# Kernel tuning notes

Hardware: AMD Instinct MI355X
Metric: run time of the kernel (lower is better)

The kernel has to match this reference:

```python
import jax, jax.numpy as jnp
import numpy as np

B, D, N_CLASSES = 8192, 256, 64
MARGIN = 0.5


def setup_inputs() -> dict:
    key = jax.random.key(0)
    k1, k2 = jax.random.split(key)
    emb = jax.random.normal(k1, (B, D), dtype=jnp.float32)
    emb = emb / jnp.linalg.norm(emb, axis=1, keepdims=True)  # module expects L2-normalised
    labels = jax.random.randint(k2, (B,), 0, N_CLASSES)
    return {"embeddings": emb, "labels": labels}


def _pairwise_dist(x):
    # torch.cdist(x, x, p=2): sqrt of clamped squared distances, safe at 0 for grads
    sq = jnp.sum(x * x, axis=1)
    d2 = jnp.maximum(sq[:, None] + sq[None, :] - 2.0 * (x @ x.T), 0.0)
    safe = jnp.where(d2 > 0.0, d2, 1.0)
    return jnp.where(d2 > 0.0, jnp.sqrt(safe), 0.0)


def reference(embeddings, labels):
    # Vectorized semi-hard mining: for each anchor,
    #   d_ap = max positive distance; the mined negative is the MIN negative
    #   distance (argmin over the semi-hard subset == global neg argmin when
    #   that min is < d_ap + margin; otherwise the subset is empty -> skip).
    dist = _pairwise_dist(embeddings)            # [B, B]
    n = labels.shape[0]
    same = labels[:, None] == labels[None, :]
    eye = jnp.eye(n, dtype=bool)
    pos_mask = same & ~eye
    neg_mask = ~same

    NEG = jnp.float32(-1e30)
    POS = jnp.float32(1e30)
    d_ap = jnp.max(jnp.where(pos_mask, dist, NEG), axis=1)   # hardest positive
    d_an = jnp.min(jnp.where(neg_mask, dist, POS), axis=1)   # closest negative

    has_pos = jnp.any(pos_mask, axis=1)
    has_neg = jnp.any(neg_mask, axis=1)
    valid = has_pos & has_neg & (d_an < d_ap + MARGIN)       # semi-hard exists

    losses = jax.nn.relu(d_ap - d_an + MARGIN)
    count = jnp.sum(valid)
    total = jnp.sum(jnp.where(valid, losses, 0.0))
    zero = jnp.sum(embeddings) * 0.0
    return jnp.where(count > 0, total / jnp.maximum(count, 1).astype(losses.dtype), zero)
```

## Files before the change

### kernel.cpp

```cpp
#include <hip/hip_runtime.h>
#include <hip/hip_bf16.h>

#define Bn 8192
#define Dn 256
#define MARGIN_F 0.5f

typedef short short8 __attribute__((ext_vector_type(8)));
typedef float floatx4 __attribute__((ext_vector_type(4)));

__device__ inline unsigned short f2bf(float f) {
    unsigned int u = __float_as_uint(f);
    unsigned int r = (u + 0x7fffu + ((u >> 16) & 1u)) >> 16;
    return (unsigned short)r;
}

#define OFF_SQ   ((size_t)Bn * Dn * 2)
#define OFF_POS  (OFF_SQ + Bn * 4)
#define OFF_NEG  (OFF_POS + Bn * 4)
#define OFF_ACC  (OFF_NEG + Bn * 4)

__global__ __launch_bounds__(256) void prep_kernel(
        const float* __restrict__ emb, unsigned short* __restrict__ embT,
        float* __restrict__ sq, unsigned int* __restrict__ posb,
        unsigned int* __restrict__ negb, unsigned int* __restrict__ accs) {
    const int w = threadIdx.x >> 6;
    const int lane = threadIdx.x & 63;
    const int row = blockIdx.x * 4 + w;

    const float4 v = *(const float4*)(emb + (size_t)row * Dn + lane * 4);
    float ss = v.x * v.x + v.y * v.y + v.z * v.z + v.w * v.w;
    #pragma unroll
    for (int m = 32; m >= 1; m >>= 1) ss += __shfl_xor(ss, m);

    uint2 o;
    o.x = (unsigned int)f2bf(v.x) | ((unsigned int)f2bf(v.y) << 16);
    o.y = (unsigned int)f2bf(v.z) | ((unsigned int)f2bf(v.w) << 16);
    const int kg = lane >> 1;
    *(uint2*)(embT + ((size_t)kg * Bn + row) * 8 + (lane & 1) * 4) = o;

    if (lane == 0) {
        sq[row] = ss;
        posb[row] = 0u;
        negb[row] = 0xFFFFFFFFu;
    }
    if (blockIdx.x == 0 && threadIdx.x == 0) {
        accs[0] = 0u; accs[1] = 0u; accs[2] = 0u;
    }
}

__global__ __launch_bounds__(256, 2) void mine_kernel(
        const unsigned short* __restrict__ embT, const float* __restrict__ sq,
        const int* __restrict__ labels, unsigned int* __restrict__ posb,
        unsigned int* __restrict__ negb) {
    const int tid  = threadIdx.x;
    const int w    = tid >> 6;
    const int lane = tid & 63;
    const int quad = lane >> 4;
    const int c    = lane & 15;

    const int iBase  = blockIdx.x * 256 + w * 64;
    const int jSplit = blockIdx.y * 512;

    const size_t KS = (size_t)4 * Bn * 8;

    short8 aFrag[4][8];
    #pragma unroll
    for (int m = 0; m < 4; ++m) {
        const unsigned short* ap = embT + ((size_t)quad * Bn + iBase + m * 16 + c) * 8;
        #pragma unroll
        for (int ks = 0; ks < 8; ++ks)
            aFrag[m][ks] = *(const short8*)(ap + ks * KS);
    }
    int labI[4][4];
    #pragma unroll
    for (int m = 0; m < 4; ++m)
        #pragma unroll
        for (int r = 0; r < 4; ++r)
            labI[m][r] = labels[iBase + m * 16 + quad * 4 + r];

    float rpos[4][4], rneg[4][4];
    #pragma unroll
    for (int m = 0; m < 4; ++m)
        #pragma unroll
        for (int r = 0; r < 4; ++r) { rpos[m][r] = -1e30f; rneg[m][r] = 1e30f; }

    for (int jt = 0; jt < 16; ++jt) {
        #pragma unroll
        for (int n = 0; n < 2; ++n) {
            const int jRow = jSplit + jt * 32 + n * 16 + c;
            const unsigned short* bp = embT + ((size_t)quad * Bn + jRow) * 8;
            const float sj = sq[jRow];
            const int   lj = labels[jRow];
            floatx4 acc[4];
            #pragma unroll
            for (int m = 0; m < 4; ++m) acc[m] = (floatx4){0.f, 0.f, 0.f, 0.f};
            #pragma unroll
            for (int kc = 0; kc < 2; ++kc) {
                short8 bF[4];
                #pragma unroll
                for (int k4 = 0; k4 < 4; ++k4)
                    bF[k4] = *(const short8*)(bp + (kc * 4 + k4) * KS);
                #pragma unroll
                for (int k4 = 0; k4 < 4; ++k4)
                    #pragma unroll
                    for (int m = 0; m < 4; ++m)
                        acc[m] = __builtin_amdgcn_mfma_f32_16x16x32_bf16(
                            aFrag[m][kc * 4 + k4], bF[k4], acc[m], 0, 0, 0);
            }
            #pragma unroll
            for (int m = 0; m < 4; ++m)
                #pragma unroll
                for (int r = 0; r < 4; ++r) {
                    float s = fmaf(-2.0f, acc[m][r], sj);
                    bool  e = (lj == labI[m][r]);
                    rpos[m][r] = e ? fmaxf(rpos[m][r], s) : rpos[m][r];
                    rneg[m][r] = e ? rneg[m][r] : fminf(rneg[m][r], s);
                }
        }
    }

    #pragma unroll
    for (int m = 0; m < 4; ++m)
        #pragma unroll
        for (int r = 0; r < 4; ++r) {
            float p = rpos[m][r], q = rneg[m][r];
            #pragma unroll
            for (int msk = 1; msk <= 8; msk <<= 1) {
                p = fmaxf(p, __shfl_xor(p, msk));
                q = fminf(q, __shfl_xor(q, msk));
            }
            if (c == 0) {
                int ig = iBase + m * 16 + quad * 4 + r;
                if (p > -1e29f) atomicMax(&posb[ig], __float_as_uint(p + 4.0f));
                if (q <  1e29f) atomicMin(&negb[ig], __float_as_uint(q + 4.0f));
            }
        }
}

__global__ __launch_bounds__(256) void finalize_kernel(
        const float* __restrict__ sq, const unsigned int* __restrict__ posb,
        const unsigned int* __restrict__ negb, float* __restrict__ accsF,
        unsigned int* __restrict__ accsU, float* __restrict__ out) {
    const int i = blockIdx.x * 256 + threadIdx.x;
    unsigned int pb = posb[i], nb = negb[i];
    bool hp = (pb != 0u);
    bool hn = (nb != 0xFFFFFFFFu);
    float si  = sq[i];
    float dap = sqrtf(fmaxf(si + (__uint_as_float(pb) - 4.0f), 0.0f));
    float dan = sqrtf(fmaxf(si + (__uint_as_float(nb) - 4.0f), 0.0f));
    bool valid = hp && hn && (dan < dap + MARGIN_F);
    float t  = valid ? fmaxf(dap - dan + MARGIN_F, 0.0f) : 0.0f;
    float cc = valid ? 1.0f : 0.0f;
    #pragma unroll
    for (int m = 32; m >= 1; m >>= 1) {
        t  += __shfl_xor(t, m);
        cc += __shfl_xor(cc, m);
    }
    __shared__ float sT[4], sC[4];
    int w = threadIdx.x >> 6, lane = threadIdx.x & 63;
    if (lane == 0) { sT[w] = t; sC[w] = cc; }
    __syncthreads();
    if (threadIdx.x == 0) {
        atomicAdd(&accsF[0], sT[0] + sT[1] + sT[2] + sT[3]);
        atomicAdd(&accsF[1], sC[0] + sC[1] + sC[2] + sC[3]);
        __threadfence();
        unsigned int ticket = atomicAdd(&accsU[2], 1u);
        if (ticket == gridDim.x - 1) {
            float tot = atomicAdd(&accsF[0], 0.0f);
            float cnt = atomicAdd(&accsF[1], 0.0f);
            out[0] = (cnt > 0.0f) ? tot / cnt : 0.0f;
        }
    }
}

extern "C" void kernel_launch(void* const* d_in, const int* in_sizes, int n_in,
                              void* d_out, int out_size, void* d_ws, size_t ws_size,
                              hipStream_t stream) {
    const float* emb   = (const float*)d_in[0];
    const int*  labels = (const int*)d_in[1];
    float* out = (float*)d_out;

    char* ws = (char*)d_ws;
    unsigned short* embT = (unsigned short*)ws;
    float*        sqv  = (float*)(ws + OFF_SQ);
    unsigned int* posb = (unsigned int*)(ws + OFF_POS);
    unsigned int* negb = (unsigned int*)(ws + OFF_NEG);
    float*        accsF = (float*)(ws + OFF_ACC);
    unsigned int* accsU = (unsigned int*)(ws + OFF_ACC);

    prep_kernel<<<Bn / 4, 256, 0, stream>>>(emb, embT, sqv, posb, negb, accsU);
    mine_kernel<<<dim3(32, 16), 256, 0, stream>>>(embT, sqv, labels, posb, negb);
    finalize_kernel<<<Bn / 256, 256, 0, stream>>>(sqv, posb, negb, accsF, accsU, out);
}
```

Baseline: 119.8 us.

## Stage B tiles in LDS via async global_load_lds with double buffering

```diff
diff --git a/kernel.cpp b/kernel.cpp
--- a/kernel.cpp
+++ b/kernel.cpp
@@ -48,7 +48,7 @@
     }
 }
 
-__global__ __launch_bounds__(256, 2) void mine_kernel(
+__global__ __launch_bounds__(256, 3) void mine_kernel(
         const unsigned short* __restrict__ embT, const float* __restrict__ sq,
         const int* __restrict__ labels, unsigned int* __restrict__ posb,
         unsigned int* __restrict__ negb) {
@@ -58,69 +58,86 @@
     const int quad = lane >> 4;
     const int c    = lane & 15;
 
-    const int iBase  = blockIdx.x * 256 + w * 64;
-    const int jSplit = blockIdx.y * 512;
+    const int iBase = blockIdx.x * 128 + w * 32;
+    const int jBase = blockIdx.y * 512;
 
     const size_t KS = (size_t)4 * Bn * 8;
 
-    short8 aFrag[4][8];
-    #pragma unroll
-    for (int m = 0; m < 4; ++m) {
+    __shared__ __align__(16) unsigned short Bt[2][32 * 32 * 8];
+
+    short8 aFrag[2][8];
+    #pragma unroll
+    for (int m = 0; m < 2; ++m) {
         const unsigned short* ap = embT + ((size_t)quad * Bn + iBase + m * 16 + c) * 8;
         #pragma unroll
         for (int ks = 0; ks < 8; ++ks)
             aFrag[m][ks] = *(const short8*)(ap + ks * KS);
     }
-    int labI[4][4];
-    #pragma unroll
-    for (int m = 0; m < 4; ++m)
+    int labI[2][4];
+    #pragma unroll
+    for (int m = 0; m < 2; ++m)
         #pragma unroll
         for (int r = 0; r < 4; ++r)
             labI[m][r] = labels[iBase + m * 16 + quad * 4 + r];
 
-    float rpos[4][4], rneg[4][4];
-    #pragma unroll
-    for (int m = 0; m < 4; ++m)
+    float rpos[2][4], rneg[2][4];
+    #pragma unroll
+    for (int m = 0; m < 2; ++m)
         #pragma unroll
         for (int r = 0; r < 4; ++r) { rpos[m][r] = -1e30f; rneg[m][r] = 1e30f; }
 
+    const unsigned short* sbase = embT + ((size_t)(tid >> 5) * Bn + jBase + (tid & 31)) * 8;
+
+    #define STAGE(BUF, JT) do {                                                        \
+        const unsigned short* _s = sbase + (size_t)(JT) * 32 * 8;                      \
+        unsigned short* _d = &Bt[BUF][(size_t)tid * 8];                                \
+        _Pragma("unroll")                                                              \
+        for (int cc = 0; cc < 4; ++cc)                                                 \
+            __builtin_amdgcn_global_load_lds(                                          \
+                (const __attribute__((address_space(1))) unsigned int*)                \
+                    (_s + (size_t)cc * 8 * Bn * 8),                                    \
+                (__attribute__((address_space(3))) unsigned int*)(_d + cc * 256 * 8),  \
+                16, 0, 0);                                                             \
+    } while (0)
+
+    STAGE(0, 0);
+    __syncthreads();
+
     for (int jt = 0; jt < 16; ++jt) {
+        if (jt + 1 < 16) STAGE((jt + 1) & 1, jt + 1);
+        const unsigned short* bt = Bt[jt & 1];
         #pragma unroll
         for (int n = 0; n < 2; ++n) {
-            const int jRow = jSplit + jt * 32 + n * 16 + c;
-            const unsigned short* bp = embT + ((size_t)quad * Bn + jRow) * 8;
+            const int jRow = jBase + jt * 32 + n * 16 + c;
             const float sj = sq[jRow];
             const int   lj = labels[jRow];
-            floatx4 acc[4];
+            floatx4 acc0 = {0.f, 0.f, 0.f, 0.f};
+            floatx4 acc1 = {0.f, 0.f, 0.f, 0.f};
             #pragma unroll
-            for (int m = 0; m < 4; ++m) acc[m] = (floatx4){0.f, 0.f, 0.f, 0.f};
+            for (int ks = 0; ks < 8; ++ks) {
+                short8 bF = *(const short8*)(bt +
+                    (size_t)((ks * 4 + quad) * 32 + n * 16 + c) * 8);
+                acc0 = __builtin_amdgcn_mfma_f32_16x16x32_bf16(aFrag[0][ks], bF, acc0, 0, 0, 0);
+                acc1 = __builtin_amdgcn_mfma_f32_16x16x32_bf16(aFrag[1][ks], bF, acc1, 0, 0, 0);
+            }
             #pragma unroll
-            for (int kc = 0; kc < 2; ++kc) {
-                short8 bF[4];
-                #pragma unroll
-                for (int k4 = 0; k4 < 4; ++k4)
-                    bF[k4] = *(const short8*)(bp + (kc * 4 + k4) * KS);
-                #pragma unroll
-                for (int k4 = 0; k4 < 4; ++k4)
-                    #pragma unroll
-                    for (int m = 0; m < 4; ++m)
-                        acc[m] = __builtin_amdgcn_mfma_f32_16x16x32_bf16(
-                            aFrag[m][kc * 4 + k4], bF[k4], acc[m], 0, 0, 0);
-            }
-            #pragma unroll
-            for (int m = 0; m < 4; ++m)
-                #pragma unroll
-                for (int r = 0; r < 4; ++r) {
-                    float s = fmaf(-2.0f, acc[m][r], sj);
-                    bool  e = (lj == labI[m][r]);
-                    rpos[m][r] = e ? fmaxf(rpos[m][r], s) : rpos[m][r];
-                    rneg[m][r] = e ? rneg[m][r] : fminf(rneg[m][r], s);
-                }
+            for (int r = 0; r < 4; ++r) {
+                float s0 = fmaf(-2.0f, acc0[r], sj);
+                bool  e0 = (lj == labI[0][r]);
+                rpos[0][r] = e0 ? fmaxf(rpos[0][r], s0) : rpos[0][r];
+                rneg[0][r] = e0 ? rneg[0][r] : fminf(rneg[0][r], s0);
+                float s1 = fmaf(-2.0f, acc1[r], sj);
+                bool  e1 = (lj == labI[1][r]);
+                rpos[1][r] = e1 ? fmaxf(rpos[1][r], s1) : rpos[1][r];
+                rneg[1][r] = e1 ? rneg[1][r] : fminf(rneg[1][r], s1);
+            }
         }
-    }
-
-    #pragma unroll
-    for (int m = 0; m < 4; ++m)
+        __syncthreads();
+    }
+    #undef STAGE
+
+    #pragma unroll
+    for (int m = 0; m < 2; ++m)
         #pragma unroll
         for (int r = 0; r < 4; ++r) {
             float p = rpos[m][r], q = rneg[m][r];
@@ -189,6 +206,6 @@
     unsigned int* accsU = (unsigned int*)(ws + OFF_ACC);
 
     prep_kernel<<<Bn / 4, 256, 0, stream>>>(emb, embT, sqv, posb, negb, accsU);
-    mine_kernel<<<dim3(32, 16), 256, 0, stream>>>(embT, sqv, labels, posb, negb);
+    mine_kernel<<<dim3(64, 16), 256, 0, stream>>>(embT, sqv, labels, posb, negb);
     finalize_kernel<<<Bn / 256, 256, 0, stream>>>(sqv, posb, negb, accsF, accsU, out);
 }
```

After: 105.3 us. 1.14x faster.
